# Optimization experiments

Measured on AMD Instinct MI355X. Metric: run time of the kernel, lower is better.

Reference implementation:

```python
import jax, jax.numpy as jnp
import numpy as np

H = 16  # num_heads


def setup_inputs() -> dict:
    key = jax.random.key(0)
    ks = jax.random.split(key, 12)
    B, S, D = 2, 2048, 1024
    init = lambda k, shape: (jax.random.normal(k, shape, dtype=jnp.float32) * 0.02)
    return {
        "x": jax.random.normal(ks[0], (B, S, D), dtype=jnp.float32),
        "wq": init(ks[1], (D, D)), "bq": init(ks[2], (D,)),
        "wk": init(ks[3], (D, D)), "bk": init(ks[4], (D,)),
        "wv": init(ks[5], (D, D)), "bv": init(ks[6], (D,)),
        "wo": init(ks[7], (D, D)), "bo": init(ks[8], (D,)),
        "w3d": init(ks[9], (3, D)), "b3d": init(ks[10], (3,)),
    }


def _pairwise_l2(pos):
    # pos: [B,S,3] -> [B,S,S] Euclidean distance (safe sqrt: zero grad at 0, like torch.cdist)
    sq = jnp.sum((pos[:, :, None, :] - pos[:, None, :, :]) ** 2, axis=-1)
    safe = jnp.where(sq > 0, sq, 1.0)
    return jnp.where(sq > 0, jnp.sqrt(safe), 0.0)


def reference(x, wq, bq, wk, bk, wv, bv, wo, bo, w3d, b3d):
    B, S, D = x.shape
    hd = D // H
    scale = 1.0 / (hd ** 0.5)
    # V projection -> [B,H,S,hd]  (Q/K are computed in torch forward but unused in APPROX scores)
    V = (x @ wv.T + bv).reshape(B, S, H, hd).transpose(0, 2, 1, 3)
    # 3D semantic positions and non-dot-product scores (identical across heads)
    pos = x @ w3d.T + b3d                      # [B,S,3]
    dist = _pairwise_l2(pos)                   # [B,S,S]
    scores = -dist[:, None, :, :] * scale      # [B,H,S,S] (broadcast over heads)
    causal = jnp.triu(jnp.ones((S, S), dtype=bool), k=1)
    scores = jnp.where(causal[None, None], -jnp.inf, scores)
    attn = jax.nn.softmax(scores, axis=-1)
    attn = jnp.nan_to_num(attn, nan=0.0)
    out = jnp.einsum('bhqk,bhkd->bhqd', attn, V)  # [B,H,S,hd]
    out = out.transpose(0, 2, 1, 3).reshape(B, S, D)
    return out @ wo.T + bo
```

## Files before the change

### kernel.cpp

```cpp
#include <hip/hip_runtime.h>
#include <hip/hip_bf16.h>
#include <stdint.h>


typedef __attribute__((ext_vector_type(8))) short bf16x8;
typedef __attribute__((ext_vector_type(4))) float f32x4;
typedef __attribute__((ext_vector_type(4))) unsigned short us4;

#define AS1(p) (const __attribute__((address_space(1))) unsigned int*)(p)
#define AS3(p) (__attribute__((address_space(3))) unsigned int*)(p)

__device__ __forceinline__ unsigned short f2bf(float f) {
  union { float f; unsigned u; } v; v.f = f;
  unsigned r = v.u + 0x7FFFu + ((v.u >> 16) & 1u);
  return (unsigned short)(r >> 16);
}

__global__ void k_prep(const float* __restrict__ x, const float* __restrict__ wv,
                       const float* __restrict__ wo, const float* __restrict__ bv,
                       const float* __restrict__ bo, const float* __restrict__ w3d,
                       const float* __restrict__ b3d,
                       unsigned short* __restrict__ xT, unsigned short* __restrict__ wvT,
                       unsigned short* __restrict__ wob, float* __restrict__ cvec,
                       float* __restrict__ pos) {
  __shared__ __align__(16) float lsm[64 * 68];
  const int bx = blockIdx.x, t = threadIdx.x;
  if (bx < 1024) {
    const int b = bx >> 9, rest = bx & 511, st = rest >> 4, dt = rest & 15;
    const int s0 = st * 64, d0 = dt * 64;
    const int r = t >> 2, c4 = t & 3;
    const float* src = x + (size_t)(b * 2048 + s0 + r) * 1024 + d0;
    float (*ld)[68] = (float(*)[68])lsm;
    #pragma unroll
    for (int p = 0; p < 4; p++)
      *(float4*)&ld[r][(c4 + 4 * p) * 4] = ((const float4*)src)[c4 + 4 * p];
    __syncthreads();
    #pragma unroll
    for (int p = 0; p < 4; p++) {
      const int dl = (t >> 4) + (p << 4);
      us4 o;
      #pragma unroll
      for (int k = 0; k < 4; k++)
        ((unsigned short*)&o)[k] = f2bf(ld[(t & 15) * 4 + k][dl]);
      *(us4*)(xT + ((size_t)b << 21) + (size_t)(d0 + dl) * 2048 + s0 + (t & 15) * 4) = o;
    }
  } else if (bx < 2048) {
    const int bb = bx - 1024, tr = bb >> 5, tc = bb & 31;
    const int r = t >> 5, c = t & 31;
    float (*ld)[33] = (float(*)[33])lsm;
    #pragma unroll
    for (int rr = r; rr < 32; rr += 8)
      ld[rr][c] = wv[(size_t)(tr * 32 + rr) * 1024 + tc * 32 + c];
    __syncthreads();
    #pragma unroll
    for (int rr = r; rr < 32; rr += 8)
      wvT[(size_t)(tc * 32 + rr) * 1024 + tr * 32 + c] = f2bf(ld[c][rr]);
  } else if (bx < 3072) {
    const int oo = bx - 2048;
    const float4 w = ((const float4*)(wo + (size_t)oo * 1024))[t];
    us4 ob; ob.x = f2bf(w.x); ob.y = f2bf(w.y); ob.z = f2bf(w.z); ob.w = f2bf(w.w);
    ((us4*)(wob + (size_t)oo * 1024))[t] = ob;
    const float4 b = ((const float4*)bv)[t];
    float a = w.x * b.x + w.y * b.y + w.z * b.z + w.w * b.w;
    #pragma unroll
    for (int off = 32; off; off >>= 1) a += __shfl_down(a, off, 64);
    if ((t & 63) == 0) lsm[t >> 6] = a;
    __syncthreads();
    if (t == 0) cvec[oo] = lsm[0] + lsm[1] + lsm[2] + lsm[3] + bo[oo];
  } else {
    const int row = bx - 3072;
    const float4 xv = ((const float4*)(x + (size_t)row * 1024))[t];
    const float4 w0 = ((const float4*)(w3d))[t];
    const float4 w1 = ((const float4*)(w3d + 1024))[t];
    const float4 w2 = ((const float4*)(w3d + 2048))[t];
    float a0 = xv.x*w0.x + xv.y*w0.y + xv.z*w0.z + xv.w*w0.w;
    float a1 = xv.x*w1.x + xv.y*w1.y + xv.z*w1.z + xv.w*w1.w;
    float a2 = xv.x*w2.x + xv.y*w2.y + xv.z*w2.z + xv.w*w2.w;
    #pragma unroll
    for (int off = 32; off; off >>= 1) {
      a0 += __shfl_down(a0, off, 64);
      a1 += __shfl_down(a1, off, 64);
      a2 += __shfl_down(a2, off, 64);
    }
    if ((t & 63) == 0) { lsm[(t >> 6) * 3] = a0; lsm[(t >> 6) * 3 + 1] = a1; lsm[(t >> 6) * 3 + 2] = a2; }
    __syncthreads();
    if (t == 0) {
      pos[(size_t)row*3 + 0] = lsm[0] + lsm[3] + lsm[6] + lsm[9]  + b3d[0];
      pos[(size_t)row*3 + 1] = lsm[1] + lsm[4] + lsm[7] + lsm[10] + b3d[1];
      pos[(size_t)row*3 + 2] = lsm[2] + lsm[5] + lsm[8] + lsm[11] + b3d[2];
    }
  }
}

__global__ void k_attn(const float* __restrict__ pos, unsigned short* __restrict__ Ab) {
  const int row = blockIdx.x;
  const int q = row & 2047, bb = row >> 11;
  const float* pb = pos + ((size_t)bb << 11) * 3;
  const float qx = pb[q*3], qy = pb[q*3+1], qz = pb[q*3+2];
  const float4* pb4 = (const float4*)pb;
  const int jmax = ((q >> 7) + 1) << 7;
  float v[2][4];
  float sum = 0.f;
  #pragma unroll
  for (int cc = 0; cc < 2; cc++) {
    const int j0 = (cc << 10) + (threadIdx.x << 2);
    float e0 = 0.f, e1 = 0.f, e2 = 0.f, e3 = 0.f;
    if (j0 < jmax) {
      const float4 A4 = pb4[3*(j0 >> 2)], B4 = pb4[3*(j0 >> 2) + 1], C4 = pb4[3*(j0 >> 2) + 2];
      const float px[4] = {A4.x, A4.w, B4.z, C4.y};
      const float py[4] = {A4.y, B4.x, B4.w, C4.z};
      const float pz[4] = {A4.z, B4.y, C4.x, C4.w};
      float ee[4];
      #pragma unroll
      for (int u = 0; u < 4; u++) {
        float e = 0.f;
        if (j0 + u <= q) {
          float dx = qx - px[u], dy = qy - py[u], dz = qz - pz[u];
          float sq = fmaf(dx, dx, fmaf(dy, dy, dz*dz));
          float d = sq > 0.f ? sqrtf(sq) : 0.f;
          e = __expf(-0.125f * d);
        }
        ee[u] = e;
      }
      e0 = ee[0]; e1 = ee[1]; e2 = ee[2]; e3 = ee[3];
    }
    v[cc][0] = e0; v[cc][1] = e1; v[cc][2] = e2; v[cc][3] = e3;
    sum += e0 + e1 + e2 + e3;
  }
  #pragma unroll
  for (int off = 32; off; off >>= 1) sum += __shfl_down(sum, off, 64);
  __shared__ float red[4];
  if ((threadIdx.x & 63) == 0) red[threadIdx.x >> 6] = sum;
  __syncthreads();
  const float inv = 1.f / (red[0] + red[1] + red[2] + red[3]);
  unsigned short* orow = Ab + (size_t)row * 2048;
  #pragma unroll
  for (int cc = 0; cc < 2; cc++) {
    const int j0 = (cc << 10) + (threadIdx.x << 2);
    if (j0 < jmax) {
      us4 o;
      o.x = f2bf(v[cc][0]*inv); o.y = f2bf(v[cc][1]*inv);
      o.z = f2bf(v[cc][2]*inv); o.w = f2bf(v[cc][3]*inv);
      *(us4*)(orow + j0) = o;
    }
  }
}

template<int BM, int BN, int WM, int WN>
__device__ __forceinline__ void gemm_loop(
    const unsigned short* __restrict__ A, int lda,
    const unsigned short* __restrict__ Bt, int ldb,
    int m0, int n0, int kmax,
    unsigned short* lds, f32x4* acc) {
  constexpr int WAVES = WM * WN;
  constexpr int FI = BM / (WM * 16), FJ = BN / (WN * 16);
  constexpr int CPW = ((BM + BN) / 8) / WAVES;
  constexpr int BUFSZ = (BM + BN) * 64;
  const int tid = threadIdx.x, l = tid & 63, w = tid >> 6;
  const int wm = w & (WM - 1), wn = w / WM;
  const int gcol = ((l & 7) ^ (l >> 3)) << 3;

  auto stage = [&](int buf, int k0) {
    unsigned short* base = lds + buf * BUFSZ;
    #pragma unroll
    for (int e = 0; e < CPW; ++e) {
      const int c = w * CPW + e;
      const unsigned short* src;
      unsigned short* dst;
      if (c < BM / 8) {
        src = A + (size_t)(m0 + c*8 + (l >> 3)) * lda + k0 + gcol;
        dst = base + c * 512;
      } else {
        const int cb = c - BM / 8;
        src = Bt + (size_t)(n0 + cb*8 + (l >> 3)) * ldb + k0 + gcol;
        dst = base + BM * 64 + cb * 512;
      }
      __builtin_amdgcn_global_load_lds(AS1(src), AS3(dst), 16, 0, 0);
    }
  };

  auto compute = [&](int buf) {
    unsigned short* lA = lds + buf * BUFSZ;
    unsigned short* lB = lA + BM * 64;
    #pragma unroll
    for (int h = 0; h < 2; ++h) {
      const int slot = ((h << 2) | (l >> 4)) ^ (l & 7);
      bf16x8 af[FI], bfr[FJ];
      #pragma unroll
      for (int i = 0; i < FI; ++i) {
        const int ar = wm * (BM / WM) + i * 16 + (l & 15);
        af[i] = *(const bf16x8*)&lA[ar * 64 + slot * 8];
      }
      #pragma unroll
      for (int j = 0; j < FJ; ++j) {
        const int br = wn * (BN / WN) + j * 16 + (l & 15);
        bfr[j] = *(const bf16x8*)&lB[br * 64 + slot * 8];
      }
      #pragma unroll
      for (int i = 0; i < FI; ++i)
        #pragma unroll
        for (int j = 0; j < FJ; ++j)
          acc[i * FJ + j] = __builtin_amdgcn_mfma_f32_16x16x32_bf16(af[i], bfr[j], acc[i * FJ + j], 0, 0, 0);
    }
  };

  const int NT = kmax >> 6;
  stage(0, 0);
  if (NT > 1) stage(1, 64);
  int cur = 0, nxt2 = 2;
  for (int t = 0; t < NT; ++t) {
    if (t < NT - 1) {
      static_assert(CPW == 4 || CPW == 6 || CPW == 8, "vmcnt literal");
      if constexpr (CPW == 4) asm volatile("s_waitcnt vmcnt(4) lgkmcnt(0)" ::: "memory");
      else if constexpr (CPW == 6) asm volatile("s_waitcnt vmcnt(6) lgkmcnt(0)" ::: "memory");
      else asm volatile("s_waitcnt vmcnt(8) lgkmcnt(0)" ::: "memory");
    } else {
      asm volatile("s_waitcnt vmcnt(0) lgkmcnt(0)" ::: "memory");
    }
    __builtin_amdgcn_s_barrier();
    if (t + 2 < NT) stage(nxt2, (t + 2) << 6);
    compute(cur);
    cur = cur == 2 ? 0 : cur + 1;
    nxt2 = nxt2 == 2 ? 0 : nxt2 + 1;
  }
}

__global__ __launch_bounds__(256, 2) void k_gemm_axwc(
    const unsigned short* __restrict__ Ab, const unsigned short* __restrict__ xT,
    unsigned short* __restrict__ Axb,
    const unsigned short* __restrict__ wob, const unsigned short* __restrict__ wvT,
    unsigned short* __restrict__ Wcs) {
  __shared__ __align__(16) unsigned short lds[3 * (128 + 64) * 64];
  const int bx = blockIdx.x;
  const int l = threadIdx.x & 63, w = threadIdx.x >> 6;
  const int wm = w & 1, wn = w >> 1;
  if (bx < 512) {
    f32x4 acc[8] = {};
    const int xcd = bx & 7, rest = bx >> 3;
    const int g = rest >> 4, n0i = rest & 15;
    const int mi = (g < 2) ? (15 - xcd) : xcd;
    const int b = g & 1;
    const int m0 = mi << 7, n0 = n0i << 6;
    const unsigned short* A  = Ab + ((size_t)b << 22);
    const unsigned short* Bt = xT + ((size_t)b << 21);
    gemm_loop<128, 64, 2, 2>(A, 2048, Bt, 2048, m0, n0, (mi + 1) << 7, lds, acc);
    unsigned short* Obase = Axb + ((size_t)b << 11) * 1024;
    #pragma unroll
    for (int i = 0; i < 4; i++) {
      const int r0 = m0 + wm*64 + i*16 + ((l >> 4) << 2);
      #pragma unroll
      for (int j = 0; j < 2; j++) {
        const int cidx = n0 + wn*32 + j*16 + (l & 15);
        #pragma unroll
        for (int t = 0; t < 4; t++)
          Obase[(size_t)(r0 + t) * 1024 + cidx] = f2bf(acc[i*2 + j][t]);
      }
    }
  } else {
    f32x4 acc[4] = {};
    const int g = bx - 512;
    const int m0 = (g & 15) * 64, n0 = (g >> 4) * 64;
    gemm_loop<64, 64, 2, 2>(wob, 1024, wvT, 1024, m0, n0, 1024, lds, acc);
    #pragma unroll
    for (int i = 0; i < 2; i++) {
      const int r0 = m0 + wm*32 + i*16 + ((l >> 4) << 2);
      #pragma unroll
      for (int j = 0; j < 2; j++) {
        const int cidx = n0 + wn*32 + j*16 + (l & 15);
        #pragma unroll
        for (int t = 0; t < 4; t++)
          Wcs[(size_t)(r0 + t) * 1024 + cidx] = f2bf(acc[i*2 + j][t]);
      }
    }
  }
}

__global__ __launch_bounds__(256, 2) void k_gemm_out(
    const unsigned short* __restrict__ Axb, const unsigned short* __restrict__ Wcs,
    const float* __restrict__ cvec, float* __restrict__ out) {
  __shared__ __align__(16) unsigned short lds[3 * (128 + 64) * 64];
  f32x4 acc[8] = {};
  const int m0 = blockIdx.x * 128, n0 = blockIdx.y * 64;
  gemm_loop<128, 64, 2, 2>(Axb, 1024, Wcs, 1024, m0, n0, 1024, lds, acc);
  const int l = threadIdx.x & 63, w = threadIdx.x >> 6;
  const int wm = w & 1, wn = w >> 1;
  #pragma unroll
  for (int i = 0; i < 4; i++) {
    const int r0 = m0 + wm*64 + i*16 + ((l >> 4) << 2);
    #pragma unroll
    for (int j = 0; j < 2; j++) {
      const int cidx = n0 + wn*32 + j*16 + (l & 15);
      const float cv = cvec[cidx];
      #pragma unroll
      for (int t = 0; t < 4; t++)
        out[(size_t)(r0 + t) * 1024 + cidx] = acc[i*2 + j][t] + cv;
    }
  }
}

extern "C" void kernel_launch(void* const* d_in, const int* in_sizes, int n_in,
                              void* d_out, int out_size, void* d_ws, size_t ws_size,
                              hipStream_t stream) {
  const float* x   = (const float*)d_in[0];
  const float* wv  = (const float*)d_in[5];
  const float* bv  = (const float*)d_in[6];
  const float* wo  = (const float*)d_in[7];
  const float* bo  = (const float*)d_in[8];
  const float* w3d = (const float*)d_in[9];
  const float* b3d = (const float*)d_in[10];
  float* out = (float*)d_out;

  char* ws = (char*)d_ws;
  unsigned short* xT  = (unsigned short*)(ws);
  unsigned short* wvT = (unsigned short*)(ws + ( 8u << 20));
  unsigned short* wob = (unsigned short*)(ws + (10u << 20));
  unsigned short* Wcs = (unsigned short*)(ws + (12u << 20));
  unsigned short* Axb = (unsigned short*)(ws + (14u << 20));
  unsigned short* Ab  = (unsigned short*)(ws + (22u << 20));
  float*          pos = (float*)(ws + (38u << 20));
  float*          cvec= (float*)(ws + (39u << 20));

  k_prep<<<7168, 256, 0, stream>>>(x, wv, wo, bv, bo, w3d, b3d, xT, wvT, wob, cvec, pos);
  k_attn<<<4096, 256, 0, stream>>>(pos, Ab);
  k_gemm_axwc<<<768, 256, 0, stream>>>(Ab, xT, Axb, wob, wvT, Wcs);
  k_gemm_out<<<dim3(32, 16), 256, 0, stream>>>(Axb, Wcs, cvec, out);
}
```

Measured before the change: 56.74 us.

## Stage positions in LDS per attention block and retile output GEMM

The attention-weight kernel now launches 512 blocks. Each block loads the whole batch's positions into shared memory once, stored as separate x/y/z arrays, and processes 8 query rows strided by 256. This replaces per-row global loads with vectorized LDS reads and balances the causal work across blocks. The output GEMM switches from 128x64 tiles on a 2x2 wave grid to 64x128 tiles on a 1x4 wave grid, with a 1D grid whose block order walks the N tiles first. Fewer attention blocks lowers parallelism and adds a sync per row, and the staging uses about 24KB of LDS per block.

```diff
diff --git a/kernel.cpp b/kernel.cpp
--- a/kernel.cpp
+++ b/kernel.cpp
@@ -93,61 +93,73 @@
 }
 
 __global__ void k_attn(const float* __restrict__ pos, unsigned short* __restrict__ Ab) {
-  const int row = blockIdx.x;
-  const int q = row & 2047, bb = row >> 11;
-  const float* pb = pos + ((size_t)bb << 11) * 3;
-  const float qx = pb[q*3], qy = pb[q*3+1], qz = pb[q*3+2];
-  const float4* pb4 = (const float4*)pb;
-  const int jmax = ((q >> 7) + 1) << 7;
-  float v[2][4];
-  float sum = 0.f;
-  #pragma unroll
-  for (int cc = 0; cc < 2; cc++) {
-    const int j0 = (cc << 10) + (threadIdx.x << 2);
-    float e0 = 0.f, e1 = 0.f, e2 = 0.f, e3 = 0.f;
-    if (j0 < jmax) {
-      const float4 A4 = pb4[3*(j0 >> 2)], B4 = pb4[3*(j0 >> 2) + 1], C4 = pb4[3*(j0 >> 2) + 2];
-      const float px[4] = {A4.x, A4.w, B4.z, C4.y};
-      const float py[4] = {A4.y, B4.x, B4.w, C4.z};
-      const float pz[4] = {A4.z, B4.y, C4.x, C4.w};
-      float ee[4];
-      #pragma unroll
-      for (int u = 0; u < 4; u++) {
-        float e = 0.f;
-        if (j0 + u <= q) {
-          float dx = qx - px[u], dy = qy - py[u], dz = qz - pz[u];
-          float sq = fmaf(dx, dx, fmaf(dy, dy, dz*dz));
-          float d = sq > 0.f ? sqrtf(sq) : 0.f;
-          e = __expf(-0.125f * d);
+  __shared__ __align__(16) float sp[3 * 2048 + 4];
+  const int bid = blockIdx.x, t = threadIdx.x;
+  const int b = bid >> 8, r0 = bid & 255;
+  const float* pb = pos + ((size_t)b << 11) * 3;
+  for (int idx = t; idx < 6144; idx += 256) {
+    const float val = pb[idx];
+    const int row = idx / 3, comp = idx - row * 3;
+    sp[comp * 2048 + row] = val;
+  }
+  float* red = sp + 6144;
+  __syncthreads();
+  for (int k = 0; k < 8; ++k) {
+    const int q = r0 + (k << 8);
+    const float qx = sp[q], qy = sp[2048 + q], qz = sp[4096 + q];
+    const int jmax = ((q >> 7) + 1) << 7;
+    float v[2][4];
+    float sum = 0.f;
+    #pragma unroll
+    for (int cc = 0; cc < 2; cc++) {
+      const int j0 = (cc << 10) + (t << 2);
+      float e0 = 0.f, e1 = 0.f, e2 = 0.f, e3 = 0.f;
+      if (j0 < jmax) {
+        const float4 px4 = *(const float4*)&sp[j0];
+        const float4 py4 = *(const float4*)&sp[2048 + j0];
+        const float4 pz4 = *(const float4*)&sp[4096 + j0];
+        const float px[4] = {px4.x, px4.y, px4.z, px4.w};
+        const float py[4] = {py4.x, py4.y, py4.z, py4.w};
+        const float pz[4] = {pz4.x, pz4.y, pz4.z, pz4.w};
+        float ee[4];
+        #pragma unroll
+        for (int u = 0; u < 4; u++) {
+          float e = 0.f;
+          if (j0 + u <= q) {
+            float dx = qx - px[u], dy = qy - py[u], dz = qz - pz[u];
+            float sq = fmaf(dx, dx, fmaf(dy, dy, dz*dz));
+            float d = sq > 0.f ? sqrtf(sq) : 0.f;
+            e = __expf(-0.125f * d);
+          }
+          ee[u] = e;
         }
-        ee[u] = e;
-      }
-      e0 = ee[0]; e1 = ee[1]; e2 = ee[2]; e3 = ee[3];
-    }
-    v[cc][0] = e0; v[cc][1] = e1; v[cc][2] = e2; v[cc][3] = e3;
-    sum += e0 + e1 + e2 + e3;
-  }
-  #pragma unroll
-  for (int off = 32; off; off >>= 1) sum += __shfl_down(sum, off, 64);
-  __shared__ float red[4];
-  if ((threadIdx.x & 63) == 0) red[threadIdx.x >> 6] = sum;
-  __syncthreads();
-  const float inv = 1.f / (red[0] + red[1] + red[2] + red[3]);
-  unsigned short* orow = Ab + (size_t)row * 2048;
-  #pragma unroll
-  for (int cc = 0; cc < 2; cc++) {
-    const int j0 = (cc << 10) + (threadIdx.x << 2);
-    if (j0 < jmax) {
-      us4 o;
-      o.x = f2bf(v[cc][0]*inv); o.y = f2bf(v[cc][1]*inv);
-      o.z = f2bf(v[cc][2]*inv); o.w = f2bf(v[cc][3]*inv);
-      *(us4*)(orow + j0) = o;
-    }
+        e0 = ee[0]; e1 = ee[1]; e2 = ee[2]; e3 = ee[3];
+      }
+      v[cc][0] = e0; v[cc][1] = e1; v[cc][2] = e2; v[cc][3] = e3;
+      sum += e0 + e1 + e2 + e3;
+    }
+    #pragma unroll
+    for (int off = 32; off; off >>= 1) sum += __shfl_down(sum, off, 64);
+    if ((t & 63) == 0) red[t >> 6] = sum;
+    __syncthreads();
+    const float inv = 1.f / (red[0] + red[1] + red[2] + red[3]);
+    unsigned short* orow = Ab + ((size_t)(b * 2048 + q)) * 2048;
+    #pragma unroll
+    for (int cc = 0; cc < 2; cc++) {
+      const int j0 = (cc << 10) + (t << 2);
+      if (j0 < jmax) {
+        us4 o;
+        o.x = f2bf(v[cc][0]*inv); o.y = f2bf(v[cc][1]*inv);
+        o.z = f2bf(v[cc][2]*inv); o.w = f2bf(v[cc][3]*inv);
+        *(us4*)(orow + j0) = o;
+      }
+    }
+    __syncthreads();
   }
 }
 
 template<int BM, int BN, int WM, int WN>
-__device__ __forceinline__ void gemm_loop(
+__device__ __forceinline__ void gemm_ring(
     const unsigned short* __restrict__ A, int lda,
     const unsigned short* __restrict__ Bt, int ldb,
     int m0, int n0, int kmax,
@@ -243,7 +255,7 @@
     const int m0 = mi << 7, n0 = n0i << 6;
     const unsigned short* A  = Ab + ((size_t)b << 22);
     const unsigned short* Bt = xT + ((size_t)b << 21);
-    gemm_loop<128, 64, 2, 2>(A, 2048, Bt, 2048, m0, n0, (mi + 1) << 7, lds, acc);
+    gemm_ring<128, 64, 2, 2>(A, 2048, Bt, 2048, m0, n0, (mi + 1) << 7, lds, acc);
     unsigned short* Obase = Axb + ((size_t)b << 11) * 1024;
     #pragma unroll
     for (int i = 0; i < 4; i++) {
@@ -260,7 +272,7 @@
     f32x4 acc[4] = {};
     const int g = bx - 512;
     const int m0 = (g & 15) * 64, n0 = (g >> 4) * 64;
-    gemm_loop<64, 64, 2, 2>(wob, 1024, wvT, 1024, m0, n0, 1024, lds, acc);
+    gemm_ring<64, 64, 2, 2>(wob, 1024, wvT, 1024, m0, n0, 1024, lds, acc);
     #pragma unroll
     for (int i = 0; i < 2; i++) {
       const int r0 = m0 + wm*32 + i*16 + ((l >> 4) << 2);
@@ -278,18 +290,18 @@
 __global__ __launch_bounds__(256, 2) void k_gemm_out(
     const unsigned short* __restrict__ Axb, const unsigned short* __restrict__ Wcs,
     const float* __restrict__ cvec, float* __restrict__ out) {
-  __shared__ __align__(16) unsigned short lds[3 * (128 + 64) * 64];
+  __shared__ __align__(16) unsigned short lds[3 * (64 + 128) * 64];
   f32x4 acc[8] = {};
-  const int m0 = blockIdx.x * 128, n0 = blockIdx.y * 64;
-  gemm_loop<128, 64, 2, 2>(Axb, 1024, Wcs, 1024, m0, n0, 1024, lds, acc);
+  const int bid = blockIdx.x;
+  const int n0 = (bid & 7) * 128, m0 = (bid >> 3) * 64;
+  gemm_ring<64, 128, 1, 4>(Axb, 1024, Wcs, 1024, m0, n0, 1024, lds, acc);
   const int l = threadIdx.x & 63, w = threadIdx.x >> 6;
-  const int wm = w & 1, wn = w >> 1;
   #pragma unroll
   for (int i = 0; i < 4; i++) {
-    const int r0 = m0 + wm*64 + i*16 + ((l >> 4) << 2);
+    const int r0 = m0 + i*16 + ((l >> 4) << 2);
     #pragma unroll
     for (int j = 0; j < 2; j++) {
-      const int cidx = n0 + wn*32 + j*16 + (l & 15);
+      const int cidx = n0 + w*32 + j*16 + (l & 15);
       const float cv = cvec[cidx];
       #pragma unroll
       for (int t = 0; t < 4; t++)
@@ -321,7 +333,7 @@
   float*          cvec= (float*)(ws + (39u << 20));
 
   k_prep<<<7168, 256, 0, stream>>>(x, wv, wo, bv, bo, w3d, b3d, xT, wvT, wob, cvec, pos);
-  k_attn<<<4096, 256, 0, stream>>>(pos, Ab);
+  k_attn<<<512, 256, 0, stream>>>(pos, Ab);
   k_gemm_axwc<<<768, 256, 0, stream>>>(Ab, xT, Axb, wob, wvT, Wcs);
-  k_gemm_out<<<dim3(32, 16), 256, 0, stream>>>(Axb, Wcs, cvec, out);
-}
+  k_gemm_out<<<512, 256, 0, stream>>>(Axb, Wcs, cvec, out);
+}
```

Result: slower. 63.43 us (+11.8%).
